# Performance work log

Measured on AMD Instinct MI355X. Metric: run time of the kernel, lower is better.

## Reference

```python
import jax, jax.numpy as jnp
import numpy as np

B, C, H, W = 4, 256, 64, 64
GROUPS = 32
EPS = 1e-6
N_BITS_QKV = 8
N_BITS_SM = 8


def setup_inputs() -> dict:
    key = jax.random.key(0)
    ks = jax.random.split(key, 6)
    s = 1.0 / np.sqrt(C)
    return {
        "x": jax.random.normal(ks[0], (B, C, H, W), jnp.float32),
        "gn_scale": jnp.ones((C,), jnp.float32),
        "gn_bias": jnp.zeros((C,), jnp.float32),
        "wq": jax.random.normal(ks[1], (C, C), jnp.float32) * s,
        "bq": jnp.zeros((C,), jnp.float32),
        "wk": jax.random.normal(ks[2], (C, C), jnp.float32) * s,
        "bk": jnp.zeros((C,), jnp.float32),
        "wv": jax.random.normal(ks[3], (C, C), jnp.float32) * s,
        "bv": jnp.zeros((C,), jnp.float32),
        "wproj": jax.random.normal(ks[4], (C, C), jnp.float32) * s,
        "bproj": jnp.zeros((C,), jnp.float32),
        # per-tensor uniform-affine quantizer params (delta, zero_point)
        "dq": jnp.float32(8.0 / 255.0), "zq": jnp.float32(128.0),
        "dk": jnp.float32(8.0 / 255.0), "zk": jnp.float32(128.0),
        "dv": jnp.float32(8.0 / 255.0), "zv": jnp.float32(128.0),
        "dw": jnp.float32(1.0 / 255.0), "zw": jnp.float32(0.0),
    }


def ste_round(x):
    # round with straight-through gradient (as in round_ste of BRECQ/QDrop)
    return x + jax.lax.stop_gradient(jnp.round(x) - x)


def fake_quant(x, delta, zero_point, n_bits):
    # UniformAffineQuantizer: quant -> clamp -> dequant
    n_levels = 2 ** n_bits
    x_int = ste_round(x / delta) + zero_point
    x_q = jnp.clip(x_int, 0, n_levels - 1)
    return (x_q - zero_point) * delta


def group_norm(x, scale, bias):
    b, c, h, w = x.shape
    xg = x.reshape(b, GROUPS, (c // GROUPS) * h * w)
    mu = xg.mean(-1, keepdims=True)
    var = xg.var(-1, keepdims=True)
    xn = ((xg - mu) * jax.lax.rsqrt(var + EPS)).reshape(b, c, h, w)
    return xn * scale[None, :, None, None] + bias[None, :, None, None]


def conv1x1(x, w, b):
    # 1x1 conv == channel-mixing matmul
    return jnp.einsum('bchw,oc->bohw', x, w) + b[None, :, None, None]


def reference(x, gn_scale, gn_bias, wq, bq, wk, bk, wv, bv, wproj, bproj,
              dq, zq, dk, zk, dv, zv, dw, zw):
    h_ = group_norm(x, gn_scale, gn_bias)
    q = conv1x1(h_, wq, bq)
    k = conv1x1(h_, wk, bk)
    v = conv1x1(h_, wv, bv)
    b, c, h, w = q.shape
    hw = h * w
    q = q.reshape(b, c, hw).transpose(0, 2, 1)   # [b, hw, c]
    k = k.reshape(b, c, hw)                      # [b, c, hw]
    q = fake_quant(q, dq, zq, N_BITS_QKV)
    k = fake_quant(k, dk, zk, N_BITS_QKV)
    attn = jnp.einsum('bnc,bcm->bnm', q, k) * (c ** -0.5)  # [b, hw, hw]
    attn = jax.nn.softmax(attn, axis=2)
    v = fake_quant(v.reshape(b, c, hw), dv, zv, N_BITS_QKV)
    attn = fake_quant(attn.transpose(0, 2, 1), dw, zw, N_BITS_SM)  # [b, m, n]
    h_out = jnp.einsum('bcm,bmn->bcn', v, attn).reshape(b, c, h, w)
    return x + conv1x1(h_out, wproj, bproj)
```

## Files before the change

### kernel.cpp

```cpp
#include <hip/hip_runtime.h>


#define Bb 4
#define Cc 256
#define Nn 4096
#define NGRP 32
#define LOG2E 1.4426950408889634f

typedef unsigned short u16;
typedef unsigned int   u32;
typedef unsigned char  u8;
typedef __attribute__((ext_vector_type(8))) short bf16x8;
typedef __attribute__((ext_vector_type(4))) float f32x4;
typedef __attribute__((ext_vector_type(4))) int   i32x4;

#define MFMA16(a,b,c)    __builtin_amdgcn_mfma_f32_16x16x32_bf16((a),(b),(c),0,0,0)
#define MFMA_I8(a,b,c)   __builtin_amdgcn_mfma_i32_16x16x64_i8((a),(b),(c),0,0,0)

static __device__ __forceinline__ u16 f2bf(float x){
  u32 u = __float_as_uint(x);
  u += 0x7fffu + ((u >> 16) & 1u);
  return (u16)(u >> 16);
}
static __device__ __forceinline__ float bf2f(u16 h){ return __uint_as_float(((u32)h) << 16); }

union U64c { u16 u[4]; uint2 v; };

__global__ __launch_bounds__(256) void k_gn_stats(const float* __restrict__ x,
                                                  float* __restrict__ mu, float* __restrict__ rs){
  int bg = blockIdx.x;
  const float4* p = (const float4*)(x + (size_t)bg * (8 * Nn));
  float s = 0.f, q = 0.f;
  for (int i = threadIdx.x; i < 8*Nn/4; i += 256){
    float4 v = p[i];
    s += v.x + v.y + v.z + v.w;
    q += v.x*v.x + v.y*v.y + v.z*v.z + v.w*v.w;
  }
  __shared__ float rsum[256], rsq[256];
  rsum[threadIdx.x] = s; rsq[threadIdx.x] = q;
  __syncthreads();
  for (int off = 128; off > 0; off >>= 1){
    if (threadIdx.x < off){ rsum[threadIdx.x] += rsum[threadIdx.x+off]; rsq[threadIdx.x] += rsq[threadIdx.x+off]; }
    __syncthreads();
  }
  if (threadIdx.x == 0){
    const float inv = 1.0f / (8*Nn);
    float m = rsum[0]*inv;
    float var = rsq[0]*inv - m*m;
    mu[bg] = m; rs[bg] = rsqrtf(var + 1e-6f);
  }
}

__global__ __launch_bounds__(256) void k_wsplit(const float* __restrict__ wq, const float* __restrict__ wk,
                                                const float* __restrict__ wv, const float* __restrict__ wp,
                                                u16* __restrict__ WH, u16* __restrict__ WL){
  int gid = blockIdx.x*256 + threadIdx.x;
  int mat = gid >> 16, idx = gid & 65535;
  const float* src = (mat == 0) ? wq : (mat == 1) ? wk : (mat == 2) ? wv : wp;
  float w = src[idx];
  u16 h = f2bf(w);
  WH[gid] = h;
  WL[gid] = f2bf(w - bf2f(h));
}

__global__ __launch_bounds__(256) void k_gn_apply(const float* __restrict__ x,
                                                  const float* __restrict__ gsc, const float* __restrict__ gbi,
                                                  const float* __restrict__ mu, const float* __restrict__ rs,
                                                  u16* __restrict__ hhi, u16* __restrict__ hlo){
  int nt = blockIdx.x, ct = blockIdx.y, b = blockIdx.z;
  int n0 = nt*64, c0 = ct*64;
  __shared__ float yt[64*65];
  __shared__ float sa[64], sb[64];
  int t = threadIdx.x;
  if (t < 64){
    int c = c0 + t;
    int bg = b*NGRP + (c >> 3);
    float a = rs[bg] * gsc[c];
    sa[t] = a;
    sb[t] = gbi[c] - mu[bg]*a;
  }
  __syncthreads();
  #pragma unroll
  for (int j = 0; j < 4; ++j){
    int id = t + j*256;
    int r = id >> 4, cq = id & 15;
    float4 v = *(const float4*)(x + ((size_t)b*Cc + c0 + r)*Nn + n0 + cq*4);
    float a = sa[r], bb = sb[r];
    yt[r*65 + cq*4 + 0] = v.x*a + bb;
    yt[r*65 + cq*4 + 1] = v.y*a + bb;
    yt[r*65 + cq*4 + 2] = v.z*a + bb;
    yt[r*65 + cq*4 + 3] = v.w*a + bb;
  }
  __syncthreads();
  int nl = t >> 2, cg = (t & 3) * 16;
  size_t base = ((size_t)b*Nn + n0 + nl)*Cc + c0 + cg;
  #pragma unroll
  for (int half = 0; half < 2; ++half){
    union { u16 u[8]; uint4 v; } Ph, Pl;
    #pragma unroll
    for (int u = 0; u < 8; ++u){
      float y = yt[(cg + half*8 + u)*65 + nl];
      u16 h = f2bf(y);
      Ph.u[u] = h; Pl.u[u] = f2bf(y - bf2f(h));
    }
    *(uint4*)(hhi + base + half*8) = Ph.v;
    *(uint4*)(hlo + base + half*8) = Pl.v;
  }
}

__global__ __launch_bounds__(256) void k_convqkv(const u16* __restrict__ WH, const u16* __restrict__ WL,
                                                 const u16* __restrict__ Hhi, const u16* __restrict__ Hlo,
                                                 const float* __restrict__ bq, const float* __restrict__ bk,
                                                 const float* __restrict__ bv,
                                                 const float* __restrict__ dq, const float* __restrict__ zq,
                                                 const float* __restrict__ dk, const float* __restrict__ zk,
                                                 const float* __restrict__ dv, const float* __restrict__ zv,
                                                 u8* __restrict__ qT8, u8* __restrict__ kT8,
                                                 u8* __restrict__ v8){
  int nt = blockIdx.x, ot = blockIdx.y, b = blockIdx.z;
  __shared__ u16 Lh[64*256], Ll[64*256];
  int t = threadIdx.x, lane = t & 63, wave = t >> 6;
  int lo16 = lane & 15, quad = lane >> 4;
  int o0 = ot*64 + wave*16;

  {
    const u16* hb = Hhi + ((size_t)b*Nn + nt*64) * 256;
    const u16* lb = Hlo + ((size_t)b*Nn + nt*64) * 256;
    #pragma unroll
    for (int j = 0; j < 8; ++j){
      int id = t + j*256;
      int r = id >> 5, ch = id & 31;
      int sw = (ch ^ (r & 15)) * 8;
      *(uint4*)(Lh + r*256 + sw) = *(const uint4*)(hb + (size_t)r*256 + ch*8);
      *(uint4*)(Ll + r*256 + sw) = *(const uint4*)(lb + (size_t)r*256 + ch*8);
    }
  }
  __syncthreads();

  const float* Bs[3] = {bq, bk, bv};
  const float* Dsr[3] = {dq, dk, dv};
  const float* Zs[3] = {zq, zk, zv};

  #pragma unroll
  for (int ws = 0; ws < 3; ++ws){
    bf16x8 awh[8], awl[8];
    {
      const u16* wbh = WH + (size_t)ws*65536 + (size_t)(o0 + lo16) * 256 + quad*8;
      const u16* wbl = WL + (size_t)ws*65536 + (size_t)(o0 + lo16) * 256 + quad*8;
      #pragma unroll
      for (int k = 0; k < 8; ++k){
        awh[k] = *(const bf16x8*)(wbh + k*32);
        awl[k] = *(const bf16x8*)(wbl + k*32);
      }
    }
    f32x4 zf = {0.f,0.f,0.f,0.f};
    f32x4 acc[4] = {zf, zf, zf, zf};
    #pragma unroll
    for (int k = 0; k < 8; ++k){
      #pragma unroll
      for (int ns = 0; ns < 4; ++ns){
        int r = ns*16 + lo16;
        int ph = ((k*4 + quad) ^ (r & 15)) * 8;
        bf16x8 bh = *(const bf16x8*)(Lh + r*256 + ph);
        bf16x8 bl = *(const bf16x8*)(Ll + r*256 + ph);
        acc[ns] = MFMA16(awh[k], bh, acc[ns]);
        acc[ns] = MFMA16(awl[k], bh, acc[ns]);
        acc[ns] = MFMA16(awh[k], bl, acc[ns]);
      }
    }
    float bia[4];
    #pragma unroll
    for (int r = 0; r < 4; ++r) bia[r] = Bs[ws][o0 + quad*4 + r];
    float z = Zs[ws][0]; float invd = 1.0f / Dsr[ws][0];

    if (ws < 2){
      u8* outT = (ws == 0) ? qT8 : kT8;
      #pragma unroll
      for (int ns = 0; ns < 4; ++ns){
        int n = nt*64 + ns*16 + lo16;
        u32 w = 0;
        #pragma unroll
        for (int r = 0; r < 4; ++r){
          float v = acc[ns][r] + bia[r];
          float xq = fminf(fmaxf(rintf(v*invd) + z, 0.f), 255.f);
          int qi = (int)rintf(xq - z);
          w |= ((u32)(qi & 255)) << (8*r);
        }
        *(u32*)(outT + ((size_t)b*Nn + n)*Cc + o0 + quad*4) = w;
      }
    } else {
      #pragma unroll
      for (int ns = 0; ns < 4; ++ns){
        int n = nt*64 + ns*16 + lo16;
        #pragma unroll
        for (int r = 0; r < 4; ++r){
          float v = acc[ns][r] + bia[r];
          float xq = fminf(fmaxf(rintf(v*invd) + z, 0.f), 255.f);
          int qi = (int)rintf(xq - z);
          v8[((size_t)b*Cc + o0 + quad*4 + r)*Nn + n] = (u8)(qi & 255);
        }
      }
    }
  }
}

__global__ __launch_bounds__(256) void k_conv(const u16* __restrict__ WH, const u16* __restrict__ WL,
                                              const u16* __restrict__ Hh,
                                              const float* __restrict__ bias,
                                              const float* __restrict__ xres, float* __restrict__ outF){
  int nt = blockIdx.x, ot = blockIdx.y, b = blockIdx.z;
  __shared__ u16 Lh[64*128];
  int t = threadIdx.x, lane = t & 63, wave = t >> 6;
  int lo16 = lane & 15, quad = lane >> 4;
  int o0 = ot*64 + wave*16;

  bf16x8 awh[8], awl[8];
  {
    const u16* wbh = WH + (size_t)3*65536 + (size_t)(o0 + lo16) * 256 + quad*8;
    const u16* wbl = WL + (size_t)3*65536 + (size_t)(o0 + lo16) * 256 + quad*8;
    #pragma unroll
    for (int k = 0; k < 8; ++k){
      awh[k] = *(const bf16x8*)(wbh + k*32);
      awl[k] = *(const bf16x8*)(wbl + k*32);
    }
  }
  f32x4 zf = {0.f,0.f,0.f,0.f};
  f32x4 acc[4] = {zf, zf, zf, zf};

  const u16* hb = Hh + ((size_t)b*Nn + nt*64) * 256;
  for (int kc = 0; kc < 2; ++kc){
    __syncthreads();
    for (int id = t; id < 64*16; id += 256){
      int r = id >> 4, ch = id & 15;
      int sw = (ch ^ (r & 7)) * 8;
      *(uint4*)(Lh + r*128 + sw) = *(const uint4*)(hb + (size_t)r*256 + kc*128 + ch*8);
    }
    __syncthreads();
    #pragma unroll
    for (int k4 = 0; k4 < 4; ++k4){
      int k = kc*4 + k4;
      #pragma unroll
      for (int ns = 0; ns < 4; ++ns){
        int r = ns*16 + lo16;
        int ch = ((k4*4 + quad) ^ (r & 7)) * 8;
        bf16x8 bh = *(const bf16x8*)(Lh + r*128 + ch);
        acc[ns] = MFMA16(awh[k], bh, acc[ns]);
        acc[ns] = MFMA16(awl[k], bh, acc[ns]);
      }
    }
  }

  float bia[4];
  #pragma unroll
  for (int r = 0; r < 4; ++r) bia[r] = bias[o0 + quad*4 + r];
  #pragma unroll
  for (int ns = 0; ns < 4; ++ns){
    int n = nt*64 + ns*16 + lo16;
    #pragma unroll
    for (int r = 0; r < 4; ++r){
      size_t a = ((size_t)b*Cc + o0 + quad*4 + r)*Nn + n;
      outF[a] = xres[a] + acc[ns][r] + bia[r];
    }
  }
}

static __device__ __forceinline__ void stage64x256(u8* dst, const u8* __restrict__ src, int t){
  #pragma unroll
  for (int j = 0; j < 4; ++j){
    int id = t + j*256; int r = id >> 4, ch = id & 15;
    *(uint4*)(dst + r*256 + ((ch ^ (r & 15)) << 4)) = *(const uint4*)(src + r*256 + ch*16);
  }
}

static __device__ __forceinline__ int sq4(u32 w){
  int s = 0;
  #pragma unroll
  for (int j = 0; j < 4; ++j){ int v = (int)((signed char)((w >> (8*j)) & 0xffu)); s += v*v; }
  return s;
}
static __device__ __forceinline__ int ssum4(u32 w){
  return ((int)(w << 24) >> 24) + ((int)(w << 16) >> 24) + ((int)(w << 8) >> 24) + ((int)w >> 24);
}
__global__ __launch_bounds__(256) void k_normvs(const u8* __restrict__ qT8, const u8* __restrict__ kT8,
                                                const u8* __restrict__ v8,
                                                u32* __restrict__ stat, int* __restrict__ vsum){
  if (blockIdx.x < 128){
    int gid = blockIdx.x*256 + threadIdx.x;
    int which = gid >> 14;
    int rid = gid & 16383;
    const u8* row = (which ? kT8 : qT8) + (size_t)rid * 256;
    u32 acc = 0;
    const uint4* p = (const uint4*)row;
    #pragma unroll
    for (int i = 0; i < 16; ++i){
      uint4 w = p[i];
      acc += (u32)(sq4(w.x) + sq4(w.y) + sq4(w.z) + sq4(w.w));
    }
    #pragma unroll
    for (int msk = 32; msk > 0; msk >>= 1){
      u32 o = (u32)__shfl_xor((int)acc, msk, 64);
      acc = acc > o ? acc : o;
    }
    if ((threadIdx.x & 63) == 0)
      atomicMax(&stat[which*4 + (rid >> 12)], acc);
  } else {
    int row = blockIdx.x - 128;
    uint4 w = *(const uint4*)(v8 + (size_t)row*Nn + threadIdx.x*16);
    int s = ssum4(w.x) + ssum4(w.y) + ssum4(w.z) + ssum4(w.w);
    #pragma unroll
    for (int msk = 1; msk < 64; msk <<= 1) s += __shfl_xor(s, msk, 64);
    __shared__ int r4[4];
    if ((threadIdx.x & 63) == 0) r4[threadIdx.x >> 6] = s;
    __syncthreads();
    if (threadIdx.x == 0) vsum[row] = r4[0] + r4[1] + r4[2] + r4[3];
  }
}

__global__ __launch_bounds__(256) void k_sumexp(const u8* __restrict__ qT8, const u8* __restrict__ kT8,
                                                const u32* __restrict__ stat,
                                                const float* __restrict__ pdq, const float* __restrict__ pdk,
                                                float* __restrict__ Lp){
  int nt = blockIdx.x, mc = blockIdx.y, b = blockIdx.z;
  __shared__ u8 Kt[64*256];
  int t = threadIdx.x, lane = t & 63, wave = t >> 6;
  int lo16 = lane & 15, quad = lane >> 4;

  i32x4 a[4];
  {
    const u8* qb = qT8 + ((size_t)b*Nn + nt*64)*256;
    int ar = wave*16 + lo16;
    #pragma unroll
    for (int k = 0; k < 4; ++k)
      a[k] = *(const i32x4*)(qb + ar*256 + (k*4 + quad)*16);
  }
  float sc2 = pdq[0]*pdk[0]*0.0625f*LOG2E;
  float M2 = sc2 * sqrtf((float)stat[b] * (float)stat[4+b]);
  float lr[4] = {0.f,0.f,0.f,0.f};

  const u8* kbase = kT8 + ((size_t)b*Nn + mc*512)*256;
  for (int mt = 0; mt < 8; ++mt){
    __syncthreads();
    stage64x256(Kt, kbase + (size_t)mt*64*256, t);
    __syncthreads();
    #pragma unroll
    for (int ms = 0; ms < 4; ++ms){
      i32x4 acc = {0,0,0,0};
      int br = ms*16 + lo16;
      #pragma unroll
      for (int k = 0; k < 4; ++k){
        i32x4 bk_ = *(const i32x4*)(Kt + br*256 + (((k*4 + quad) ^ (br & 15)) << 4));
        acc = MFMA_I8(a[k], bk_, acc);
      }
      #pragma unroll
      for (int r = 0; r < 4; ++r)
        lr[r] += exp2f(fmaf((float)acc[r], sc2, -M2));
    }
  }
  #pragma unroll
  for (int msk = 1; msk < 16; msk <<= 1){
    #pragma unroll
    for (int r = 0; r < 4; ++r) lr[r] += __shfl_xor(lr[r], msk, 64);
  }
  if (lo16 == 0){
    #pragma unroll
    for (int r = 0; r < 4; ++r)
      Lp[((size_t)(b*8 + mc))*Nn + nt*64 + wave*16 + quad*4 + r] = lr[r];
  }
}

__global__ __launch_bounds__(256) void k_quant(const u8* __restrict__ qT8, const u8* __restrict__ kT8,
                                               const u32* __restrict__ stat,
                                               const float* __restrict__ pdq, const float* __restrict__ pdk,
                                               const float* __restrict__ pdw, const float* __restrict__ pzw,
                                               const float* __restrict__ Lp,
                                               u8* __restrict__ aqB){
  int nt = blockIdx.x, mc = blockIdx.y, b = blockIdx.z;
  __shared__ u8 Kt[64*256];
  __shared__ u32 Wb[64*16];
  int t = threadIdx.x, lane = t & 63, wave = t >> 6;
  int lo16 = lane & 15, quad = lane >> 4;

  i32x4 a[4];
  {
    const u8* qb = qT8 + ((size_t)b*Nn + nt*64)*256;
    int ar = wave*16 + lo16;
    #pragma unroll
    for (int k = 0; k < 4; ++k)
      a[k] = *(const i32x4*)(qb + ar*256 + (k*4 + quad)*16);
  }
  float sc2 = pdq[0]*pdk[0]*0.0625f*LOG2E;
  float M2 = sc2 * sqrtf((float)stat[b] * (float)stat[4+b]);
  float invdw = 1.0f / pdw[0];
  float zw = pzw[0];
  int n0 = nt*64 + wave*16 + quad*4;
  float4 Ls = {0.f,0.f,0.f,0.f};
  #pragma unroll
  for (int mcc = 0; mcc < 8; ++mcc){
    float4 v = *(const float4*)(Lp + ((size_t)(b*8 + mcc))*Nn + n0);
    Ls.x += v.x; Ls.y += v.y; Ls.z += v.z; Ls.w += v.w;
  }
  float cr[4] = { __log2f(invdw/Ls.x) - M2, __log2f(invdw/Ls.y) - M2,
                  __log2f(invdw/Ls.z) - M2, __log2f(invdw/Ls.w) - M2 };
  u32 bsel = (u32)(lane & 3);
  u32 sel1 = 0x0C0C0000u | ((4u + bsel) << 8) | bsel;

  const u8* kbase = kT8 + ((size_t)b*Nn + mc*512)*256;
  for (int mt = 0; mt < 8; ++mt){
    __syncthreads();
    stage64x256(Kt, kbase + (size_t)mt*64*256, t);
    __syncthreads();
    #pragma unroll
    for (int ms = 0; ms < 4; ++ms){
      i32x4 acc = {0,0,0,0};
      int br = ms*16 + lo16;
      #pragma unroll
      for (int k = 0; k < 4; ++k){
        i32x4 bk_ = *(const i32x4*)(Kt + br*256 + (((k*4 + quad) ^ (br & 15)) << 4));
        acc = MFMA_I8(a[k], bk_, acc);
      }
      u32 w = 0;
      #pragma unroll
      for (int r = 0; r < 4; ++r){
        float at = exp2f(fmaf((float)acc[r], sc2, cr[r]));
        float y = fminf(fmaxf(rintf(at) + zw, 0.f), 255.f);
        w = __builtin_amdgcn_cvt_pk_u8_f32(y, (u32)r, w);
      }
      int mloc = ms*16 + lo16;
      Wb[mloc*16 + ((wave*4 + quad) ^ (mloc & 15))] = w ^ 0x80808080u;
    }
    __syncthreads();
    {
      int mrow = wave*16;
      u32 ww[16];
      #pragma unroll
      for (int j = 0; j < 16; ++j)
        ww[j] = Wb[(mrow + j)*16 + (((u32)(lane >> 2)) ^ (u32)j)];
      uint4 o;
      {
        u32 p01 = __builtin_amdgcn_perm(ww[1],  ww[0],  sel1);
        u32 p23 = __builtin_amdgcn_perm(ww[3],  ww[2],  sel1);
        o.x = __builtin_amdgcn_perm(p23, p01, 0x05040100u);
        u32 p45 = __builtin_amdgcn_perm(ww[5],  ww[4],  sel1);
        u32 p67 = __builtin_amdgcn_perm(ww[7],  ww[6],  sel1);
        o.y = __builtin_amdgcn_perm(p67, p45, 0x05040100u);
        u32 p89 = __builtin_amdgcn_perm(ww[9],  ww[8],  sel1);
        u32 pab = __builtin_amdgcn_perm(ww[11], ww[10], sel1);
        o.z = __builtin_amdgcn_perm(pab, p89, 0x05040100u);
        u32 pcd = __builtin_amdgcn_perm(ww[13], ww[12], sel1);
        u32 pef = __builtin_amdgcn_perm(ww[15], ww[14], sel1);
        o.w = __builtin_amdgcn_perm(pef, pcd, 0x05040100u);
      }
      size_t mch = (size_t)(mc*32 + mt*4 + wave);
      *(uint4*)(aqB + (size_t)b*Nn*Nn + (mch*Nn + nt*64 + lane)*16) = o;
    }
  }
}

__global__ __launch_bounds__(256) void k_pv(const u8* __restrict__ v8, const u8* __restrict__ aqB,
                                            const int* __restrict__ vsum,
                                            const float* __restrict__ pdv, const float* __restrict__ pdw,
                                            const float* __restrict__ pzw,
                                            u16* __restrict__ h2){
  int nt = blockIdx.x, ct = blockIdx.y, b = blockIdx.z;
  __shared__ u8 Vt[2][64*64];
  __shared__ u8 At[2][256*16];
  int t = threadIdx.x, lane = t & 63, wave = t >> 6;
  int lo16 = lane & 15, quad = lane >> 4;

  i32x4 zi = {0,0,0,0};
  i32x4 acc[4] = {zi,zi,zi,zi};

  int vc = t >> 2, vch = t & 3;
  const u8* vrow = v8 + ((size_t)(b*Cc + ct*64 + vc))*Nn + vch*16;
  const u8* abase = aqB + (size_t)b*Nn*Nn + ((size_t)nt*64 + lane)*16;
  int vofs = (vc*64 + ((vch ^ ((vc >> 1) & 3)) << 4));
  int aofs = (wave*64 + lane)*16;

  uint4 vreg = *(const uint4*)(vrow);
  uint4 areg = *(const uint4*)(abase + (size_t)wave*Nn*16);

  for (int mt = 0; mt < 64; ++mt){
    int buf = mt & 1;
    *(uint4*)(Vt[buf] + vofs) = vreg;
    *(uint4*)(At[buf] + aofs) = areg;
    __syncthreads();
    if (mt < 63){
      vreg = *(const uint4*)(vrow + (mt+1)*64);
      areg = *(const uint4*)(abase + (size_t)((mt+1)*4 + wave)*Nn*16);
    }
    int cr = wave*16 + lo16;
    i32x4 af = *(const i32x4*)(Vt[buf] + cr*64 + ((quad ^ ((cr >> 1) & 3)) << 4));
    #pragma unroll
    for (int ns = 0; ns < 4; ++ns){
      i32x4 bf_ = *(const i32x4*)(At[buf] + (quad*64 + ns*16 + lo16)*16);
      acc[ns] = MFMA_I8(af, bf_, acc[ns]);
    }
  }
  float s = pdv[0] * pdw[0];
  float corr = s * (128.0f - pzw[0]);
  int c0 = ct*64 + wave*16 + quad*4;
  float cv[4];
  #pragma unroll
  for (int r = 0; r < 4; ++r) cv[r] = corr * (float)vsum[b*Cc + c0 + r];
  #pragma unroll
  for (int ns = 0; ns < 4; ++ns){
    int n = nt*64 + ns*16 + lo16;
    U64c Uh;
    #pragma unroll
    for (int r = 0; r < 4; ++r)
      Uh.u[r] = f2bf(s*(float)acc[ns][r] + cv[r]);
    *(uint2*)(h2 + ((size_t)b*Nn + n)*Cc + c0) = Uh.v;
  }
}

extern "C" void kernel_launch(void* const* d_in, const int* in_sizes, int n_in,
                              void* d_out, int out_size, void* d_ws, size_t ws_size,
                              hipStream_t stream){
  (void)in_sizes; (void)n_in; (void)out_size; (void)ws_size;
  const float* x   = (const float*)d_in[0];
  const float* gsc = (const float*)d_in[1];
  const float* gbi = (const float*)d_in[2];
  const float* wq  = (const float*)d_in[3];
  const float* bq  = (const float*)d_in[4];
  const float* wk  = (const float*)d_in[5];
  const float* bk  = (const float*)d_in[6];
  const float* wv  = (const float*)d_in[7];
  const float* bv  = (const float*)d_in[8];
  const float* wp  = (const float*)d_in[9];
  const float* bp  = (const float*)d_in[10];
  const float* dq  = (const float*)d_in[11];
  const float* zq  = (const float*)d_in[12];
  const float* dk  = (const float*)d_in[13];
  const float* zk  = (const float*)d_in[14];
  const float* dv  = (const float*)d_in[15];
  const float* zv  = (const float*)d_in[16];
  const float* dw  = (const float*)d_in[17];
  const float* zw  = (const float*)d_in[18];
  float* out = (float*)d_out;

  const size_t SZT = (size_t)Bb*Nn*Cc;
  u16* hT_hi = (u16*)d_ws;
  u16* hT_lo = hT_hi + SZT;
  u16* h2    = hT_lo + SZT;
  u8*  qT8   = (u8*)(h2 + SZT);
  u8*  kT8   = qT8 + SZT;
  u8*  v8    = kT8 + SZT;
  u8*  aqB   = v8 + SZT;
  u16* WH    = (u16*)(aqB + (size_t)Bb*Nn*Nn);
  u16* WL    = WH + 4*65536;
  float* mu  = (float*)(WL + 4*65536);
  float* rs  = mu + 128;
  u32*  stat = (u32*)(rs + 128);
  int*  vsum = (int*)(stat + 8);
  float* Lp  = (float*)(vsum + Bb*Cc);

  k_gn_stats<<<dim3(Bb*NGRP), 256, 0, stream>>>(x, mu, rs);
  k_wsplit<<<dim3(1024), 256, 0, stream>>>(wq, wk, wv, wp, WH, WL);
  k_gn_apply<<<dim3(Nn/64, Cc/64, Bb), 256, 0, stream>>>(x, gsc, gbi, mu, rs, hT_hi, hT_lo);

  k_convqkv<<<dim3(Nn/64, 4, Bb), 256, 0, stream>>>(WH, WL, hT_hi, hT_lo,
                                                    bq, bk, bv, dq, zq, dk, zk, dv, zv,
                                                    qT8, kT8, v8);

  hipMemsetAsync(stat, 0, 8*sizeof(u32), stream);
  k_normvs<<<dim3(128 + Bb*Cc), 256, 0, stream>>>(qT8, kT8, v8, stat, vsum);
  k_sumexp<<<dim3(Nn/64, 8, Bb), 256, 0, stream>>>(qT8, kT8, stat, dq, dk, Lp);
  k_quant<<<dim3(Nn/64, 8, Bb), 256, 0, stream>>>(qT8, kT8, stat, dq, dk, dw, zw, Lp, aqB);

  k_pv<<<dim3(Nn/64, 4, Bb), 256, 0, stream>>>(v8, aqB, vsum, dv, dw, zw, h2);

  k_conv<<<dim3(Nn/64, 4, Bb), 256, 0, stream>>>(WH, WL, h2, bp, x, out);
}
```

Before: 293.2 us.

## Fuse softmax quantization and PV matmul into one flash-style kernel

Merges the kernel that computes and quantizes attention probabilities into a 4096x4096 int8 buffer with the kernel that multiplies V by that buffer. The fused kernel recomputes QK^T per 64-key tile, quantizes it into shared memory, and immediately accumulates PV, so the 64 MB attention matrix is never written to or read from global memory. The trade-off is a grid of only 256 blocks of 512 threads, with half the waves idle during the QK phase and extra barriers per tile, which may limit occupancy and overlap.

```diff
diff --git a/kernel.cpp b/kernel.cpp
--- a/kernel.cpp
+++ b/kernel.cpp
@@ -368,148 +368,121 @@
   }
 }
 
-__global__ __launch_bounds__(256) void k_quant(const u8* __restrict__ qT8, const u8* __restrict__ kT8,
-                                               const u32* __restrict__ stat,
-                                               const float* __restrict__ pdq, const float* __restrict__ pdk,
-                                               const float* __restrict__ pdw, const float* __restrict__ pzw,
-                                               const float* __restrict__ Lp,
-                                               u8* __restrict__ aqB){
-  int nt = blockIdx.x, mc = blockIdx.y, b = blockIdx.z;
-  __shared__ u8 Kt[64*256];
-  __shared__ u32 Wb[64*16];
-  int t = threadIdx.x, lane = t & 63, wave = t >> 6;
-  int lo16 = lane & 15, quad = lane >> 4;
-
-  i32x4 a[4];
-  {
-    const u8* qb = qT8 + ((size_t)b*Nn + nt*64)*256;
-    int ar = wave*16 + lo16;
-    #pragma unroll
-    for (int k = 0; k < 4; ++k)
-      a[k] = *(const i32x4*)(qb + ar*256 + (k*4 + quad)*16);
-  }
+__global__ __launch_bounds__(512) void k_qpv(const u8* __restrict__ qT8, const u8* __restrict__ kT8,
+                                             const u8* __restrict__ v8,
+                                             const u32* __restrict__ stat,
+                                             const float* __restrict__ pdq, const float* __restrict__ pdk,
+                                             const float* __restrict__ pdw, const float* __restrict__ pzw,
+                                             const float* __restrict__ Lp, const int* __restrict__ vsum,
+                                             const float* __restrict__ pdv,
+                                             u16* __restrict__ h2){
+  int nt = blockIdx.x, b = blockIdx.y;
+  __shared__ u8  Kt[64*256];
+  __shared__ u8  Vt[256*64];
+  __shared__ u32 Pt[64*16];
+  int t = threadIdx.x, lane = t & 63, w = t >> 6;
+  int lo16 = lane & 15, q = lane >> 4;
+
+  i32x4 zi = {0,0,0,0};
+  i32x4 acc[2][4] = {{zi,zi,zi,zi},{zi,zi,zi,zi}};
+
+  i32x4 qf[4];
   float sc2 = pdq[0]*pdk[0]*0.0625f*LOG2E;
   float M2 = sc2 * sqrtf((float)stat[b] * (float)stat[4+b]);
-  float invdw = 1.0f / pdw[0];
+  float crn = 0.f;
   float zw = pzw[0];
-  int n0 = nt*64 + wave*16 + quad*4;
-  float4 Ls = {0.f,0.f,0.f,0.f};
-  #pragma unroll
-  for (int mcc = 0; mcc < 8; ++mcc){
-    float4 v = *(const float4*)(Lp + ((size_t)(b*8 + mcc))*Nn + n0);
-    Ls.x += v.x; Ls.y += v.y; Ls.z += v.z; Ls.w += v.w;
-  }
-  float cr[4] = { __log2f(invdw/Ls.x) - M2, __log2f(invdw/Ls.y) - M2,
-                  __log2f(invdw/Ls.z) - M2, __log2f(invdw/Ls.w) - M2 };
-  u32 bsel = (u32)(lane & 3);
-  u32 sel1 = 0x0C0C0000u | ((4u + bsel) << 8) | bsel;
-
-  const u8* kbase = kT8 + ((size_t)b*Nn + mc*512)*256;
-  for (int mt = 0; mt < 8; ++mt){
-    __syncthreads();
-    stage64x256(Kt, kbase + (size_t)mt*64*256, t);
-    __syncthreads();
-    #pragma unroll
-    for (int ms = 0; ms < 4; ++ms){
-      i32x4 acc = {0,0,0,0};
-      int br = ms*16 + lo16;
-      #pragma unroll
-      for (int k = 0; k < 4; ++k){
-        i32x4 bk_ = *(const i32x4*)(Kt + br*256 + (((k*4 + quad) ^ (br & 15)) << 4));
-        acc = MFMA_I8(a[k], bk_, acc);
-      }
-      u32 w = 0;
-      #pragma unroll
-      for (int r = 0; r < 4; ++r){
-        float at = exp2f(fmaf((float)acc[r], sc2, cr[r]));
-        float y = fminf(fmaxf(rintf(at) + zw, 0.f), 255.f);
-        w = __builtin_amdgcn_cvt_pk_u8_f32(y, (u32)r, w);
-      }
-      int mloc = ms*16 + lo16;
-      Wb[mloc*16 + ((wave*4 + quad) ^ (mloc & 15))] = w ^ 0x80808080u;
-    }
-    __syncthreads();
-    {
-      int mrow = wave*16;
-      u32 ww[16];
-      #pragma unroll
-      for (int j = 0; j < 16; ++j)
-        ww[j] = Wb[(mrow + j)*16 + (((u32)(lane >> 2)) ^ (u32)j)];
-      uint4 o;
-      {
-        u32 p01 = __builtin_amdgcn_perm(ww[1],  ww[0],  sel1);
-        u32 p23 = __builtin_amdgcn_perm(ww[3],  ww[2],  sel1);
-        o.x = __builtin_amdgcn_perm(p23, p01, 0x05040100u);
-        u32 p45 = __builtin_amdgcn_perm(ww[5],  ww[4],  sel1);
-        u32 p67 = __builtin_amdgcn_perm(ww[7],  ww[6],  sel1);
-        o.y = __builtin_amdgcn_perm(p67, p45, 0x05040100u);
-        u32 p89 = __builtin_amdgcn_perm(ww[9],  ww[8],  sel1);
-        u32 pab = __builtin_amdgcn_perm(ww[11], ww[10], sel1);
-        o.z = __builtin_amdgcn_perm(pab, p89, 0x05040100u);
-        u32 pcd = __builtin_amdgcn_perm(ww[13], ww[12], sel1);
-        u32 pef = __builtin_amdgcn_perm(ww[15], ww[14], sel1);
-        o.w = __builtin_amdgcn_perm(pef, pcd, 0x05040100u);
-      }
-      size_t mch = (size_t)(mc*32 + mt*4 + wave);
-      *(uint4*)(aqB + (size_t)b*Nn*Nn + (mch*Nn + nt*64 + lane)*16) = o;
-    }
-  }
-}
-
-__global__ __launch_bounds__(256) void k_pv(const u8* __restrict__ v8, const u8* __restrict__ aqB,
-                                            const int* __restrict__ vsum,
-                                            const float* __restrict__ pdv, const float* __restrict__ pdw,
-                                            const float* __restrict__ pzw,
-                                            u16* __restrict__ h2){
-  int nt = blockIdx.x, ct = blockIdx.y, b = blockIdx.z;
-  __shared__ u8 Vt[2][64*64];
-  __shared__ u8 At[2][256*16];
-  int t = threadIdx.x, lane = t & 63, wave = t >> 6;
-  int lo16 = lane & 15, quad = lane >> 4;
-
-  i32x4 zi = {0,0,0,0};
-  i32x4 acc[4] = {zi,zi,zi,zi};
-
-  int vc = t >> 2, vch = t & 3;
-  const u8* vrow = v8 + ((size_t)(b*Cc + ct*64 + vc))*Nn + vch*16;
-  const u8* abase = aqB + (size_t)b*Nn*Nn + ((size_t)nt*64 + lane)*16;
-  int vofs = (vc*64 + ((vch ^ ((vc >> 1) & 3)) << 4));
-  int aofs = (wave*64 + lane)*16;
-
-  uint4 vreg = *(const uint4*)(vrow);
-  uint4 areg = *(const uint4*)(abase + (size_t)wave*Nn*16);
+  if (w < 4){
+    int n = nt*64 + w*16 + lo16;
+    const u8* qb = qT8 + ((size_t)b*Nn + n)*256;
+    #pragma unroll
+    for (int kk = 0; kk < 4; ++kk)
+      qf[kk] = *(const i32x4*)(qb + kk*64 + q*16);
+    float Ls = 0.f;
+    #pragma unroll
+    for (int mc = 0; mc < 8; ++mc) Ls += Lp[((size_t)(b*8 + mc))*Nn + n];
+    crn = __log2f(1.0f / (pdw[0] * Ls)) - M2;
+  }
+
+  int krow0 = t >> 4, krow1 = 32 + (t >> 4), kch = t & 15;
+  int vc0 = t >> 2,  vc1 = 128 + (t >> 2),  vch = t & 3;
+  const u8* kb = kT8 + ((size_t)b*Nn)*256;
+  const u8* vb = v8 + ((size_t)b*Cc)*Nn;
+  int kdst0 = krow0*256 + ((kch ^ (krow0 & 15)) << 4);
+  int kdst1 = krow1*256 + ((kch ^ (krow1 & 15)) << 4);
+  int vdst0 = vc0*64 + ((vch ^ ((vc0 >> 1) & 3)) << 4);
+  int vdst1 = vc1*64 + ((vch ^ ((vc1 >> 1) & 3)) << 4);
+
+  uint4 kr0 = *(const uint4*)(kb + (size_t)krow0*256 + kch*16);
+  uint4 kr1 = *(const uint4*)(kb + (size_t)krow1*256 + kch*16);
+  uint4 vr0 = *(const uint4*)(vb + (size_t)vc0*Nn + vch*16);
+  uint4 vr1 = *(const uint4*)(vb + (size_t)vc1*Nn + vch*16);
 
   for (int mt = 0; mt < 64; ++mt){
-    int buf = mt & 1;
-    *(uint4*)(Vt[buf] + vofs) = vreg;
-    *(uint4*)(At[buf] + aofs) = areg;
+    if (mt) __syncthreads();
+    *(uint4*)(Kt + kdst0) = kr0;
+    *(uint4*)(Kt + kdst1) = kr1;
+    *(uint4*)(Vt + vdst0) = vr0;
+    *(uint4*)(Vt + vdst1) = vr1;
     __syncthreads();
     if (mt < 63){
-      vreg = *(const uint4*)(vrow + (mt+1)*64);
-      areg = *(const uint4*)(abase + (size_t)((mt+1)*4 + wave)*Nn*16);
-    }
-    int cr = wave*16 + lo16;
-    i32x4 af = *(const i32x4*)(Vt[buf] + cr*64 + ((quad ^ ((cr >> 1) & 3)) << 4));
+      int m1 = (mt + 1) * 64;
+      kr0 = *(const uint4*)(kb + (size_t)(m1 + krow0)*256 + kch*16);
+      kr1 = *(const uint4*)(kb + (size_t)(m1 + krow1)*256 + kch*16);
+      vr0 = *(const uint4*)(vb + (size_t)vc0*Nn + m1 + vch*16);
+      vr1 = *(const uint4*)(vb + (size_t)vc1*Nn + m1 + vch*16);
+    }
+    if (w < 4){
+      int nrow = w*16 + lo16;
+      #pragma unroll
+      for (int ms = 0; ms < 4; ++ms){
+        i32x4 s = {0,0,0,0};
+        int mrow = ms*16 + lo16;
+        #pragma unroll
+        for (int kk = 0; kk < 4; ++kk){
+          i32x4 af = *(const i32x4*)(Kt + mrow*256 + (((kk*4 + q) ^ (mrow & 15)) << 4));
+          s = MFMA_I8(af, qf[kk], s);
+        }
+        u32 wp = 0;
+        #pragma unroll
+        for (int r = 0; r < 4; ++r){
+          float at = exp2f(fmaf((float)s[r], sc2, crn));
+          float y = fminf(fmaxf(rintf(at) + zw, 0.f), 255.f);
+          wp = __builtin_amdgcn_cvt_pk_u8_f32(y, (u32)r, wp);
+        }
+        Pt[nrow*16 + ((ms ^ (nrow & 3) ^ ((nrow >> 2) & 3)) << 2) + q] = wp ^ 0x80808080u;
+      }
+    }
+    __syncthreads();
+    #pragma unroll
+    for (int ct = 0; ct < 2; ++ct){
+      int cr = w*32 + ct*16 + lo16;
+      i32x4 af = *(const i32x4*)(Vt + cr*64 + ((q ^ ((cr >> 1) & 3)) << 4));
+      #pragma unroll
+      for (int ns = 0; ns < 4; ++ns){
+        int pr = ns*16 + lo16;
+        i32x4 bf_ = *(const i32x4*)(Pt + pr*16 + ((q ^ (pr & 3) ^ ((pr >> 2) & 3)) << 2));
+        acc[ct][ns] = MFMA_I8(af, bf_, acc[ct][ns]);
+      }
+    }
+  }
+
+  float s = pdv[0] * pdw[0];
+  float corr = s * (128.0f - zw);
+  #pragma unroll
+  for (int ct = 0; ct < 2; ++ct){
+    int c0 = w*32 + ct*16 + q*4;
+    float cv[4];
+    #pragma unroll
+    for (int r = 0; r < 4; ++r) cv[r] = corr * (float)vsum[b*Cc + c0 + r];
     #pragma unroll
     for (int ns = 0; ns < 4; ++ns){
-      i32x4 bf_ = *(const i32x4*)(At[buf] + (quad*64 + ns*16 + lo16)*16);
-      acc[ns] = MFMA_I8(af, bf_, acc[ns]);
-    }
-  }
-  float s = pdv[0] * pdw[0];
-  float corr = s * (128.0f - pzw[0]);
-  int c0 = ct*64 + wave*16 + quad*4;
-  float cv[4];
-  #pragma unroll
-  for (int r = 0; r < 4; ++r) cv[r] = corr * (float)vsum[b*Cc + c0 + r];
-  #pragma unroll
-  for (int ns = 0; ns < 4; ++ns){
-    int n = nt*64 + ns*16 + lo16;
-    U64c Uh;
-    #pragma unroll
-    for (int r = 0; r < 4; ++r)
-      Uh.u[r] = f2bf(s*(float)acc[ns][r] + cv[r]);
-    *(uint2*)(h2 + ((size_t)b*Nn + n)*Cc + c0) = Uh.v;
+      int n = nt*64 + ns*16 + lo16;
+      U64c Uh;
+      #pragma unroll
+      for (int r = 0; r < 4; ++r)
+        Uh.u[r] = f2bf(s*(float)acc[ct][ns][r] + cv[r]);
+      *(uint2*)(h2 + ((size_t)b*Nn + n)*Cc + c0) = Uh.v;
+    }
   }
 }
 
@@ -545,8 +518,7 @@
   u8*  qT8   = (u8*)(h2 + SZT);
   u8*  kT8   = qT8 + SZT;
   u8*  v8    = kT8 + SZT;
-  u8*  aqB   = v8 + SZT;
-  u16* WH    = (u16*)(aqB + (size_t)Bb*Nn*Nn);
+  u16* WH    = (u16*)(v8 + SZT);
   u16* WL    = WH + 4*65536;
   float* mu  = (float*)(WL + 4*65536);
   float* rs  = mu + 128;
@@ -565,9 +537,8 @@
   hipMemsetAsync(stat, 0, 8*sizeof(u32), stream);
   k_normvs<<<dim3(128 + Bb*Cc), 256, 0, stream>>>(qT8, kT8, v8, stat, vsum);
   k_sumexp<<<dim3(Nn/64, 8, Bb), 256, 0, stream>>>(qT8, kT8, stat, dq, dk, Lp);
-  k_quant<<<dim3(Nn/64, 8, Bb), 256, 0, stream>>>(qT8, kT8, stat, dq, dk, dw, zw, Lp, aqB);
-
-  k_pv<<<dim3(Nn/64, 4, Bb), 256, 0, stream>>>(v8, aqB, vsum, dv, dw, zw, h2);
+
+  k_qpv<<<dim3(Nn/64, Bb), 512, 0, stream>>>(qT8, kT8, v8, stat, dq, dk, dw, zw, Lp, vsum, dv, h2);
 
   k_conv<<<dim3(Nn/64, 4, Bb), 256, 0, stream>>>(WH, WL, h2, bp, x, out);
 }
```

New measurement: 295.1 us. Within noise of the previous version (+0.6%).
